# Kernel optimization log

Measured on AMD Instinct MI355X. Metric: run time of the kernel, lower is better.

## Reference

```python
import jax, jax.numpy as jnp
import numpy as np

N, E, D, H, C = 50000, 1600000, 128, 2, 32

def setup_inputs() -> dict:
    key = jax.random.key(0)
    ks = jax.random.split(key, 8)
    x = jax.random.normal(ks[0], (N, D), jnp.float32)
    edge_index = jax.random.randint(ks[1], (2, E), 0, N)
    intra_enrichment_weights = jax.random.uniform(ks[2], (E,), jnp.float32)
    W = jax.random.normal(ks[3], (D, H * C), jnp.float32) * (1.0 / np.sqrt(D))
    att_src = jax.random.normal(ks[4], (H, C), jnp.float32) * 0.1
    att_dst = jax.random.normal(ks[5], (H, C), jnp.float32) * 0.1
    bias = jnp.zeros((H * C,), jnp.float32)
    enrichment_scale = jnp.asarray(0.01, jnp.float32)
    return dict(x=x, edge_index=edge_index,
                intra_enrichment_weights=intra_enrichment_weights,
                W=W, att_src=att_src, att_dst=att_dst, bias=bias,
                enrichment_scale=enrichment_scale)

def reference(x, edge_index, intra_enrichment_weights, W, att_src, att_dst, bias, enrichment_scale):
    n = x.shape[0]
    xf = jax.nn.elu(x)                       # F.elu on input features
    h = (xf @ W).reshape(n, H, C)            # [N, heads, out]
    # GATConv default add_self_loops=True
    loop = jnp.arange(n, dtype=edge_index.dtype)
    src = jnp.concatenate([edge_index[0], loop])
    dst = jnp.concatenate([edge_index[1], loop])
    a_src = jnp.einsum('nhc,hc->nh', h, att_src)   # [N, H]
    a_dst = jnp.einsum('nhc,hc->nh', h, att_dst)
    alpha = jax.nn.leaky_relu(a_src[src] + a_dst[dst], 0.2)  # [E+N, H]
    # softmax over incoming edges per destination node
    m = jax.ops.segment_max(alpha, dst, num_segments=n)
    e = jnp.exp(alpha - m[dst])
    denom = jax.ops.segment_sum(e, dst, num_segments=n)
    p = e / denom[dst]                       # every node has a self-loop -> denom > 0
    out = jax.ops.segment_sum(h[src] * p[:, :, None], dst, num_segments=n)  # [N, H, C]
    out = out.reshape(n, H * C) + bias
    # enrichment bias (scatter-mean of per-edge weights over source nodes)
    s0 = edge_index[0]
    nw = jax.ops.segment_sum(intra_enrichment_weights, s0, num_segments=n)
    cnt = jax.ops.segment_sum(jnp.ones_like(intra_enrichment_weights), s0, num_segments=n)
    nw = nw / jnp.maximum(cnt, 1.0)
    nw = jnp.clip(nw, 0.2, 5.0)
    scale_factor = 0.1 * jax.nn.sigmoid(enrichment_scale)
    return out + scale_factor * (nw[:, None] - 1.0)
```

## Files before the change

kernel.cpp:

```cpp
#include <hip/hip_runtime.h>
#include <hip/hip_fp16.h>


typedef unsigned int u32;
typedef unsigned short u16;
typedef unsigned long long u64;

#define SLOTS 2432
#define NBMAX 800
#define EPB 2048

#define XS 136
#define CS 68

typedef __attribute__((ext_vector_type(8))) short short8;
typedef __attribute__((ext_vector_type(4))) float float4v;

__device__ __forceinline__ u16 f2bf(float f) {
    union { float f; u32 u; } v; v.f = f;
    u32 r = v.u + 0x7fffu + ((v.u >> 16) & 1u);
    return (u16)(r >> 16);
}
__device__ __forceinline__ float bf2f(u16 u) {
    union { u32 i; float f; } v; v.i = ((u32)u) << 16; return v.f;
}
__device__ __forceinline__ float bf_lo(u32 u) {
    union { u32 i; float f; } v; v.i = u << 16; return v.f;
}
__device__ __forceinline__ float bf_hi(u32 u) {
    union { u32 i; float f; } v; v.i = u & 0xFFFF0000u; return v.f;
}
__device__ __forceinline__ void bf_split(float v, short& hi, short& lo) {
    u16 h = f2bf(v);
    float hf = bf2f(h);
    hi = (short)h;
    lo = (short)f2bf(v - hf);
}
__device__ __forceinline__ u16 f2h(float f) {
    __half h = __float2half(f);
    return *(u16*)&h;
}
__device__ __forceinline__ float h2f(u16 u) {
    __half h = *(__half*)&u;
    return __half2float(h);
}

__global__ __launch_bounds__(256) void k_node(
    const float* __restrict__ x, const float* __restrict__ Wm,
    const float* __restrict__ att_s, const float* __restrict__ att_d,
    u32* __restrict__ hb32, float* __restrict__ a_src, float* __restrict__ a_dst,
    int* cursA, int* cursB, int nN)
{
    __shared__ __align__(16) short Ah[64 * XS];
    __shared__ __align__(16) short Al[64 * XS];
    __shared__ __align__(16) short Bh[64 * XS];
    __shared__ __align__(16) short Bl[64 * XS];
    float* Cl = (float*)Ah;

    int t = threadIdx.x;
    int n0 = blockIdx.x * 64;

    if (blockIdx.x == 0) {
        for (int i = t; i < NBMAX; i += 256) { cursA[i] = 0; cursB[i] = 0; }
    }

    {
        int f = t & 63, kq = t >> 6;
        for (int kk = 0; kk < 32; ++kk) {
            int k = kq * 32 + kk;
            float wv = Wm[k * 64 + f];
            short hi, lo; bf_split(wv, hi, lo);
            Bh[f * XS + k] = hi; Bl[f * XS + k] = lo;
        }
    }
    for (int j = 0; j < 8; ++j) {
        int idx = t + 256 * j;
        int r = idx >> 5, c4 = idx & 31;
        int gn = n0 + r;
        float4 xv = make_float4(0.f, 0.f, 0.f, 0.f);
        if (gn < nN) xv = ((const float4*)x)[(size_t)gn * 32 + c4];
        float e[4];
        e[0] = xv.x > 0.f ? xv.x : expm1f(xv.x);
        e[1] = xv.y > 0.f ? xv.y : expm1f(xv.y);
        e[2] = xv.z > 0.f ? xv.z : expm1f(xv.z);
        e[3] = xv.w > 0.f ? xv.w : expm1f(xv.w);
        short h4[4], l4[4];
#pragma unroll
        for (int i = 0; i < 4; ++i) bf_split(e[i], h4[i], l4[i]);
        *(short4*)&Ah[r * XS + c4 * 4] = make_short4(h4[0], h4[1], h4[2], h4[3]);
        *(short4*)&Al[r * XS + c4 * 4] = make_short4(l4[0], l4[1], l4[2], l4[3]);
    }
    __syncthreads();

    {
        int w = t >> 6, l = t & 63;
        int q = l >> 4, m = l & 15;
        int arow = w * 16 + m;
        float4v acc[4] = {};
#pragma unroll
        for (int ks = 0; ks < 4; ++ks) {
            int k0 = ks * 32 + q * 8;
            short8 ah = *(const short8*)&Ah[arow * XS + k0];
            short8 al = *(const short8*)&Al[arow * XS + k0];
#pragma unroll
            for (int nt = 0; nt < 4; ++nt) {
                short8 bh = *(const short8*)&Bh[(nt * 16 + m) * XS + k0];
                short8 bl = *(const short8*)&Bl[(nt * 16 + m) * XS + k0];
                acc[nt] = __builtin_amdgcn_mfma_f32_16x16x32_bf16(ah, bh, acc[nt], 0, 0, 0);
                acc[nt] = __builtin_amdgcn_mfma_f32_16x16x32_bf16(ah, bl, acc[nt], 0, 0, 0);
                acc[nt] = __builtin_amdgcn_mfma_f32_16x16x32_bf16(al, bh, acc[nt], 0, 0, 0);
            }
        }
        __syncthreads();
#pragma unroll
        for (int nt = 0; nt < 4; ++nt)
#pragma unroll
            for (int r = 0; r < 4; ++r)
                Cl[(w * 16 + q * 4 + r) * CS + nt * 16 + m] = acc[nt][r];
    }
    __syncthreads();

    {
        int nl = t >> 2, fq = t & 3;
        int gn = n0 + nl;
        float ps = 0.f, pd = 0.f;
        if (gn < nN) {
            float hv[16];
#pragma unroll
            for (int i = 0; i < 16; ++i) {
                int f = fq * 16 + i;
                hv[i] = Cl[nl * CS + f];
                ps = fmaf(hv[i], att_s[f], ps);
                pd = fmaf(hv[i], att_d[f], pd);
            }
#pragma unroll
            for (int i = 0; i < 8; ++i) {
                u32 pk = ((u32)f2bf(hv[2 * i + 1]) << 16) | (u32)f2bf(hv[2 * i]);
                hb32[(size_t)gn * 32 + fq * 8 + i] = pk;
            }
        }
        float ps2 = ps + __shfl_xor(ps, 1, 64);
        float pd2 = pd + __shfl_xor(pd, 1, 64);
        if (gn < nN && (fq & 1) == 0) {
            a_src[2 * gn + (fq >> 1)] = ps2;
            a_dst[2 * gn + (fq >> 1)] = pd2;
        }
    }
}

__global__ __launch_bounds__(512) void k_partA(
    const int* __restrict__ ei, const float* __restrict__ wgt,
    int* cursA, int* cursB, u32* bufA, u32* bufB, int E, int nb)
{
    __shared__ u32 arrA[EPB], arrB[EPB];
    __shared__ int cntA[NBMAX], cntB[NBMAX];
    __shared__ int lofsA[NBMAX], lofsB[NBMAX];
    __shared__ int basA[NBMAX], basB[NBMAX];
    __shared__ int part[512];

    int t = threadIdx.x;
    for (int b = t; b < nb; b += 512) { cntA[b] = 0; cntB[b] = 0; }
    __syncthreads();

    int base = blockIdx.x * EPB;
    int nv = min(EPB, E - base);
    int sv[4], dv[4]; float wv[4];
#pragma unroll
    for (int k = 0; k < 4; ++k) {
        int e = base + k * 512 + t;
        if (e < E) { sv[k] = ei[e]; dv[k] = ei[E + e]; wv[k] = wgt[e]; }
        else       { sv[k] = -1;    dv[k] = -1;        wv[k] = 0.f; }
    }
#pragma unroll
    for (int k = 0; k < 4; ++k) {
        if (dv[k] >= 0) {
            atomicAdd(&cntA[dv[k] >> 6], 1);
            atomicAdd(&cntB[sv[k] >> 6], 1);
        }
    }
    __syncthreads();
    for (int b = t; b < nb; b += 512) {
        int ca = cntA[b], cb = cntB[b];
        if (ca > 0) basA[b] = atomicAdd(&cursA[b], ca);
        if (cb > 0) basB[b] = atomicAdd(&cursB[b], cb);
    }
    __syncthreads();
    {
        int b0 = 2 * t, b1 = 2 * t + 1;
        int c0 = (b0 < nb) ? cntA[b0] : 0;
        int c1 = (b1 < nb) ? cntA[b1] : 0;
        part[t] = c0 + c1;
        __syncthreads();
        for (int off = 1; off < 512; off <<= 1) {
            int v = (t >= off) ? part[t - off] : 0;
            __syncthreads();
            part[t] += v;
            __syncthreads();
        }
        int ex = part[t] - (c0 + c1);
        if (b0 < nb) lofsA[b0] = ex;
        if (b1 < nb) lofsA[b1] = ex + c0;
        __syncthreads();
        c0 = (b0 < nb) ? cntB[b0] : 0;
        c1 = (b1 < nb) ? cntB[b1] : 0;
        part[t] = c0 + c1;
        __syncthreads();
        for (int off = 1; off < 512; off <<= 1) {
            int v = (t >= off) ? part[t - off] : 0;
            __syncthreads();
            part[t] += v;
            __syncthreads();
        }
        ex = part[t] - (c0 + c1);
        if (b0 < nb) lofsB[b0] = ex;
        if (b1 < nb) lofsB[b1] = ex + c0;
    }
    __syncthreads();
    for (int b = t; b < nb; b += 512) { cntA[b] = 0; cntB[b] = 0; }
    __syncthreads();
#pragma unroll
    for (int k = 0; k < 4; ++k) {
        if (dv[k] >= 0) {
            int bA = dv[k] >> 6;
            int r = lofsA[bA] + atomicAdd(&cntA[bA], 1);
            arrA[r] = ((u32)dv[k] << 16) | (u32)sv[k];
            int bB = sv[k] >> 6;
            u32 wf = (u32)(wv[k] * 65535.f);
            if (wf > 0xFFFFu) wf = 0xFFFFu;
            int r2 = lofsB[bB] + atomicAdd(&cntB[bB], 1);
            arrB[r2] = ((u32)sv[k] << 16) | wf;
        }
    }
    __syncthreads();
    for (int i = t; i < nv; i += 512) {
        u32 v = arrA[i];
        int bA = v >> 22;
        int g = basA[bA] + (i - lofsA[bA]);
        if (g < SLOTS) bufA[bA * SLOTS + g] = v;
    }
    for (int i = t; i < nv; i += 512) {
        u32 v = arrB[i];
        int bB = v >> 22;
        int g = basB[bB] + (i - lofsB[bB]);
        if (g < SLOTS) bufB[bB * SLOTS + g] = v;
    }
}

__global__ __launch_bounds__(512) void k_fused(
    const u32* __restrict__ bufA, const int* __restrict__ cursA,
    const u32* __restrict__ bufB, const int* __restrict__ cursB,
    const float* __restrict__ a_src, const float* __restrict__ a_dst,
    const u32* __restrict__ hb32, const float* __restrict__ bias,
    const float* __restrict__ esc, float* __restrict__ out, int nN)
{
    __shared__ u32 stv[SLOTS];
    __shared__ u64 rec2[SLOTS];
    __shared__ int ldeg[64], lscan[64], lcur[64];
    __shared__ float add0[64], add1[64], ass0[64], ass1[64];
    __shared__ u32 usum[64];
    __shared__ float nwl[64];

    int b = blockIdx.x, t = threadIdx.x;
    int nA = cursA[b]; if (nA > SLOTS) nA = SLOTS;
    int nB = cursB[b]; if (nB > SLOTS) nB = SLOTS;

    if (t < 64) {
        ldeg[t] = 0; lcur[t] = 0; usum[t] = 0;
        int node = (b << 6) + t;
        float2 ad = make_float2(0.f, 0.f), as = make_float2(0.f, 0.f);
        if (node < nN) {
            ad = ((const float2*)a_dst)[node];
            as = ((const float2*)a_src)[node];
        }
        add0[t] = ad.x; add1[t] = ad.y; ass0[t] = as.x; ass1[t] = as.y;
    }
    __syncthreads();

    for (int i = t; i < nA; i += 512) {
        u32 v = bufA[b * SLOTS + i];
        stv[i] = v;
        atomicAdd(&ldeg[(v >> 16) & 63], 1);
    }
    for (int i = t; i < nB; i += 512) {
        u32 v = bufB[b * SLOTS + i];
        atomicAdd(&usum[(v >> 16) & 63], 0x1000000u | (v & 0xFFFFu));
    }
    __syncthreads();

    if (t < 64) lscan[t] = ldeg[t];
    __syncthreads();
    for (int off = 1; off < 64; off <<= 1) {
        int v = 0;
        if (t < 64 && t >= off) v = lscan[t - off];
        __syncthreads();
        if (t < 64) lscan[t] += v;
        __syncthreads();
    }
    if (t < 64) {
        lscan[t] -= ldeg[t];
        u32 uv = usum[t];
        float cnt = (float)(uv >> 24);
        float nw = ((float)(uv & 0xFFFFFFu) * (1.f / 65535.f)) / fmaxf(cnt, 1.f);
        nwl[t] = fminf(fmaxf(nw, 0.2f), 5.f);
    }
    __syncthreads();

    for (int i = t; i < nA; i += 512) {
        u32 v = stv[i];
        u32 s = v & 0xFFFFu;
        int dl = (v >> 16) & 63;
        float2 ap = ((const float2*)a_src)[s];
        float v0 = ap.x + add0[dl]; v0 = v0 > 0.f ? v0 : 0.2f * v0;
        float v1 = ap.y + add1[dl]; v1 = v1 > 0.f ? v1 : 0.2f * v1;
        u32 wp = ((u32)f2h(__expf(v1)) << 16) | (u32)f2h(__expf(v0));
        int pos = lscan[dl] + atomicAdd(&lcur[dl], 1);
        rec2[pos] = ((u64)wp << 32) | (s << 7);
    }
    __syncthreads();

    int lane = t & 63, w = t >> 6;
    int l31 = lane & 31, half = lane >> 5, head = l31 >> 4;
    float sf = 0.1f / (1.f + __expf(-esc[0]));
    float2 bb = ((const float2*)bias)[l31];
    const char* hbp = (const char*)hb32 + (l31 << 2);

    for (int jj = 0; jj < 8; ++jj) {
        int j = w * 8 + jj;
        int node = (b << 6) + j;
        if (node >= nN) break;
        float t0 = ass0[j] + add0[j]; t0 = t0 > 0.f ? t0 : 0.2f * t0;
        float t1 = ass1[j] + add1[j]; t1 = t1 > 0.f ? t1 : 0.2f * t1;
        float es0 = __expf(t0), es1 = __expf(t1);
        u32 hself = *(const u32*)(hbp + ((size_t)node << 7));
        float eself = head ? es1 : es0;
        float acc0, acc1, dsum0, dsum1;
        if (half == 0) {
            acc0 = eself * bf_lo(hself); acc1 = eself * bf_hi(hself);
            dsum0 = es0; dsum1 = es1;
        } else {
            acc0 = 0.f; acc1 = 0.f; dsum0 = 0.f; dsum1 = 0.f;
        }
        int seg = lscan[j], len = ldeg[j];
        int it2 = len >> 1;
#pragma unroll 4
        for (int k = 0; k < it2; ++k) {
            u64 rec = rec2[seg + 2 * k + half];
            u32 off = (u32)rec;
            u32 wp = (u32)(rec >> 32);
            float w0 = h2f((u16)wp), w1 = h2f((u16)(wp >> 16));
            u32 hv = *(const u32*)(hbp + off);
            float wsel = head ? w1 : w0;
            acc0 = fmaf(wsel, bf_lo(hv), acc0);
            acc1 = fmaf(wsel, bf_hi(hv), acc1);
            dsum0 += w0; dsum1 += w1;
        }
        if (len & 1) {
            u64 rec = rec2[seg + len - 1];
            u32 off = (u32)rec;
            u32 wp = (u32)(rec >> 32);
            float w0 = h2f((u16)wp), w1 = h2f((u16)(wp >> 16));
            if (half) { w0 = 0.f; w1 = 0.f; }
            u32 hv = *(const u32*)(hbp + off);
            float wsel = head ? w1 : w0;
            acc0 = fmaf(wsel, bf_lo(hv), acc0);
            acc1 = fmaf(wsel, bf_hi(hv), acc1);
            dsum0 += w0; dsum1 += w1;
        }
        dsum0 += __shfl_xor(dsum0, 32, 64);
        dsum1 += __shfl_xor(dsum1, 32, 64);
        acc0  += __shfl_xor(acc0, 32, 64);
        acc1  += __shfl_xor(acc1, 32, 64);
        if (half == 0) {
            float den = head ? dsum1 : dsum0;
            float en = sf * (nwl[j] - 1.f);
            float2 o;
            o.x = acc0 / den + bb.x + en;
            o.y = acc1 / den + bb.y + en;
            ((float2*)out)[(size_t)node * 32 + l31] = o;
        }
    }
}

extern "C" void kernel_launch(void* const* d_in, const int* in_sizes, int n_in,
                              void* d_out, int out_size, void* d_ws, size_t ws_size,
                              hipStream_t stream)
{
    const float* x     = (const float*)d_in[0];
    const int*   ei    = (const int*)d_in[1];
    const float* wgt   = (const float*)d_in[2];
    const float* Wm    = (const float*)d_in[3];
    const float* att_s = (const float*)d_in[4];
    const float* att_d = (const float*)d_in[5];
    const float* bias  = (const float*)d_in[6];
    const float* esc   = (const float*)d_in[7];
    float* out = (float*)d_out;

    int nN = in_sizes[0] / 128;
    int E  = in_sizes[2];
    int NB = (nN + 63) / 64;

    char* p = (char*)d_ws;
    auto alloc = [&](size_t bytes) -> char* {
        char* r = p; p += (bytes + 255) & ~(size_t)255; return r;
    };
    u32*   hb32  = (u32*)  alloc((size_t)nN * 32 * 4);
    float* a_src = (float*)alloc((size_t)nN * 2 * 4);
    float* a_dst = (float*)alloc((size_t)nN * 2 * 4);
    int*   cursA = (int*)  alloc(NBMAX * 4);
    int*   cursB = (int*)  alloc(NBMAX * 4);
    u32*   bufA  = (u32*)  alloc((size_t)NB * SLOTS * 4);
    u32*   bufB  = (u32*)  alloc((size_t)NB * SLOTS * 4);

    int nblkA = (E + EPB - 1) / EPB;

    k_node<<<dim3((nN + 63) / 64), dim3(256), 0, stream>>>(
        x, Wm, att_s, att_d, hb32, a_src, a_dst, cursA, cursB, nN);
    k_partA<<<dim3(nblkA), dim3(512), 0, stream>>>(
        ei, wgt, cursA, cursB, bufA, bufB, E, NB);
    k_fused<<<dim3(NB), dim3(512), 0, stream>>>(
        bufA, cursA, bufB, cursB, a_src, a_dst, hb32, bias, esc, out, nN);
}
```

Baseline: 203.1 us.

## Gather four edges per wavefront with 8-byte loads, wave-shuffle scan, memset cursors

```diff
diff --git a/kernel.cpp b/kernel.cpp
--- a/kernel.cpp
+++ b/kernel.cpp
@@ -49,7 +49,7 @@
     const float* __restrict__ x, const float* __restrict__ Wm,
     const float* __restrict__ att_s, const float* __restrict__ att_d,
     u32* __restrict__ hb32, float* __restrict__ a_src, float* __restrict__ a_dst,
-    int* cursA, int* cursB, int nN)
+    int nN)
 {
     __shared__ __align__(16) short Ah[64 * XS];
     __shared__ __align__(16) short Al[64 * XS];
@@ -59,10 +59,6 @@
 
     int t = threadIdx.x;
     int n0 = blockIdx.x * 64;
-
-    if (blockIdx.x == 0) {
-        for (int i = t; i < NBMAX; i += 256) { cursA[i] = 0; cursB[i] = 0; }
-    }
 
     {
         int f = t & 63, kq = t >> 6;
@@ -156,7 +152,6 @@
     __shared__ int cntA[NBMAX], cntB[NBMAX];
     __shared__ int lofsA[NBMAX], lofsB[NBMAX];
     __shared__ int basA[NBMAX], basB[NBMAX];
-    __shared__ int part[512];
 
     int t = threadIdx.x;
     for (int b = t; b < nb; b += 512) { cntA[b] = 0; cntB[b] = 0; }
@@ -186,34 +181,25 @@
     }
     __syncthreads();
     {
-        int b0 = 2 * t, b1 = 2 * t + 1;
-        int c0 = (b0 < nb) ? cntA[b0] : 0;
-        int c1 = (b1 < nb) ? cntA[b1] : 0;
-        part[t] = c0 + c1;
-        __syncthreads();
-        for (int off = 1; off < 512; off <<= 1) {
-            int v = (t >= off) ? part[t - off] : 0;
-            __syncthreads();
-            part[t] += v;
-            __syncthreads();
-        }
-        int ex = part[t] - (c0 + c1);
-        if (b0 < nb) lofsA[b0] = ex;
-        if (b1 < nb) lofsA[b1] = ex + c0;
-        __syncthreads();
-        c0 = (b0 < nb) ? cntB[b0] : 0;
-        c1 = (b1 < nb) ? cntB[b1] : 0;
-        part[t] = c0 + c1;
-        __syncthreads();
-        for (int off = 1; off < 512; off <<= 1) {
-            int v = (t >= off) ? part[t - off] : 0;
-            __syncthreads();
-            part[t] += v;
-            __syncthreads();
-        }
-        ex = part[t] - (c0 + c1);
-        if (b0 < nb) lofsB[b0] = ex;
-        if (b1 < nb) lofsB[b1] = ex + c0;
+        int w = t >> 6, l = t & 63;
+        if (w < 2) {
+            const int* cnt = w ? cntB : cntA;
+            int* lofs = w ? lofsB : lofsA;
+            int carry = 0;
+            int nch = (nb + 63) >> 6;
+            for (int c = 0; c < nch; ++c) {
+                int b = c * 64 + l;
+                int v = (b < nb) ? cnt[b] : 0;
+                int inc = v;
+#pragma unroll
+                for (int off = 1; off < 64; off <<= 1) {
+                    int u = __shfl_up(inc, off, 64);
+                    if (l >= off) inc += u;
+                }
+                if (b < nb) lofs[b] = carry + inc - v;
+                carry += __shfl(inc, 63, 64);
+            }
+        }
     }
     __syncthreads();
     for (int b = t; b < nb; b += 512) { cntA[b] = 0; cntB[b] = 0; }
@@ -319,10 +305,12 @@
     __syncthreads();
 
     int lane = t & 63, w = t >> 6;
-    int l31 = lane & 31, half = lane >> 5, head = l31 >> 4;
+    int g = lane >> 4;
+    int f4 = lane & 15;
+    int headq = f4 >> 3;
     float sf = 0.1f / (1.f + __expf(-esc[0]));
-    float2 bb = ((const float2*)bias)[l31];
-    const char* hbp = (const char*)hb32 + (l31 << 2);
+    float4 bb = ((const float4*)bias)[f4];
+    const char* hbp = (const char*)hb32 + (f4 << 3);
 
     for (int jj = 0; jj < 8; ++jj) {
         int j = w * 8 + jj;
@@ -331,53 +319,50 @@
         float t0 = ass0[j] + add0[j]; t0 = t0 > 0.f ? t0 : 0.2f * t0;
         float t1 = ass1[j] + add1[j]; t1 = t1 > 0.f ? t1 : 0.2f * t1;
         float es0 = __expf(t0), es1 = __expf(t1);
-        u32 hself = *(const u32*)(hbp + ((size_t)node << 7));
-        float eself = head ? es1 : es0;
-        float acc0, acc1, dsum0, dsum1;
-        if (half == 0) {
-            acc0 = eself * bf_lo(hself); acc1 = eself * bf_hi(hself);
-            dsum0 = es0; dsum1 = es1;
-        } else {
-            acc0 = 0.f; acc1 = 0.f; dsum0 = 0.f; dsum1 = 0.f;
-        }
+        float a0 = 0.f, a1 = 0.f, a2 = 0.f, a3 = 0.f;
+        float ds0 = 0.f, ds1 = 0.f;
         int seg = lscan[j], len = ldeg[j];
-        int it2 = len >> 1;
+        int it = (len + 3) >> 2;
 #pragma unroll 4
-        for (int k = 0; k < it2; ++k) {
-            u64 rec = rec2[seg + 2 * k + half];
+        for (int k = 0; k < it; ++k) {
+            int e = 4 * k + g;
+            int idx = seg + (e < len ? e : len - 1);
+            u64 rec = rec2[idx];
             u32 off = (u32)rec;
             u32 wp = (u32)(rec >> 32);
             float w0 = h2f((u16)wp), w1 = h2f((u16)(wp >> 16));
-            u32 hv = *(const u32*)(hbp + off);
-            float wsel = head ? w1 : w0;
-            acc0 = fmaf(wsel, bf_lo(hv), acc0);
-            acc1 = fmaf(wsel, bf_hi(hv), acc1);
-            dsum0 += w0; dsum1 += w1;
-        }
-        if (len & 1) {
-            u64 rec = rec2[seg + len - 1];
-            u32 off = (u32)rec;
-            u32 wp = (u32)(rec >> 32);
-            float w0 = h2f((u16)wp), w1 = h2f((u16)(wp >> 16));
-            if (half) { w0 = 0.f; w1 = 0.f; }
-            u32 hv = *(const u32*)(hbp + off);
-            float wsel = head ? w1 : w0;
-            acc0 = fmaf(wsel, bf_lo(hv), acc0);
-            acc1 = fmaf(wsel, bf_hi(hv), acc1);
-            dsum0 += w0; dsum1 += w1;
-        }
-        dsum0 += __shfl_xor(dsum0, 32, 64);
-        dsum1 += __shfl_xor(dsum1, 32, 64);
-        acc0  += __shfl_xor(acc0, 32, 64);
-        acc1  += __shfl_xor(acc1, 32, 64);
-        if (half == 0) {
-            float den = head ? dsum1 : dsum0;
-            float en = sf * (nwl[j] - 1.f);
-            float2 o;
-            o.x = acc0 / den + bb.x + en;
-            o.y = acc1 / den + bb.y + en;
-            ((float2*)out)[(size_t)node * 32 + l31] = o;
-        }
+            if (e >= len) { w0 = 0.f; w1 = 0.f; }
+            u64 hv = *(const u64*)(hbp + off);
+            u32 hlo = (u32)hv, hhi = (u32)(hv >> 32);
+            float wsel = headq ? w1 : w0;
+            a0 = fmaf(wsel, bf_lo(hlo), a0);
+            a1 = fmaf(wsel, bf_hi(hlo), a1);
+            a2 = fmaf(wsel, bf_lo(hhi), a2);
+            a3 = fmaf(wsel, bf_hi(hhi), a3);
+            ds0 += w0; ds1 += w1;
+        }
+#pragma unroll
+        for (int m = 16; m <= 32; m <<= 1) {
+            a0 += __shfl_xor(a0, m, 64);
+            a1 += __shfl_xor(a1, m, 64);
+            a2 += __shfl_xor(a2, m, 64);
+            a3 += __shfl_xor(a3, m, 64);
+            ds0 += __shfl_xor(ds0, m, 64);
+            ds1 += __shfl_xor(ds1, m, 64);
+        }
+        float den0 = ds0 + es0, den1 = ds1 + es1;
+        u64 hs = *(const u64*)(hbp + ((size_t)node << 7));
+        u32 slo = (u32)hs, shi = (u32)(hs >> 32);
+        float eself = headq ? es1 : es0;
+        float den = headq ? den1 : den0;
+        float rden = 1.f / den;
+        float en = sf * (nwl[j] - 1.f);
+        float4 o;
+        o.x = (a0 + eself * bf_lo(slo)) * rden + bb.x + en;
+        o.y = (a1 + eself * bf_hi(slo)) * rden + bb.y + en;
+        o.z = (a2 + eself * bf_lo(shi)) * rden + bb.z + en;
+        o.w = (a3 + eself * bf_hi(shi)) * rden + bb.w + en;
+        if (g == 0) ((float4*)out)[(size_t)node * 16 + f4] = o;
     }
 }
 
@@ -413,8 +398,10 @@
 
     int nblkA = (E + EPB - 1) / EPB;
 
+    hipMemsetAsync(cursA, 0, NBMAX * 4, stream);
+    hipMemsetAsync(cursB, 0, NBMAX * 4, stream);
     k_node<<<dim3((nN + 63) / 64), dim3(256), 0, stream>>>(
-        x, Wm, att_s, att_d, hb32, a_src, a_dst, cursA, cursB, nN);
+        x, Wm, att_s, att_d, hb32, a_src, a_dst, nN);
     k_partA<<<dim3(nblkA), dim3(512), 0, stream>>>(
         ei, wgt, cursA, cursB, bufA, bufB, E, NB);
     k_fused<<<dim3(NB), dim3(512), 0, stream>>>(
```

New measurement: 200.5 us. No clear change (-1.3%).
